# Optimization experiments

Hardware: AMD Instinct MI355X
Metric: run time of the kernel (lower is better)

The kernel has to match this reference:

```python
import jax, jax.numpy as jnp
import numpy as np

BATCH, SEQ, D_EMBED, N_HEADS, D_HEAD = 1, 2048, 1024, 16, 64
MASK_VAL = 1e10


def setup_inputs() -> dict:
    key = jax.random.key(0)
    ks = jax.random.split(key, 5)
    s = 1.0 / np.sqrt(D_EMBED).astype(np.float32)
    return {
        "x": jax.random.normal(ks[0], (BATCH, SEQ, D_EMBED), jnp.float32),
        "W_Q": jax.random.normal(ks[1], (N_HEADS, D_HEAD, D_EMBED), jnp.float32) * s,
        "W_K": jax.random.normal(ks[2], (N_HEADS, D_HEAD, D_EMBED), jnp.float32) * s,
        "W_V": jax.random.normal(ks[3], (N_HEADS, D_HEAD, D_EMBED), jnp.float32) * s,
        "W_O": jax.random.normal(ks[4], (N_HEADS, D_EMBED, D_HEAD), jnp.float32) * s,
    }


def reference(x, W_Q, W_K, W_V, W_O):
    # x: [b, c, e] -> q,k,v: [b, a(head), c(pos), h(d_head)]
    q = jnp.einsum('ahe,bce->bach', W_Q, x)
    k = jnp.einsum('ahe,bce->bach', W_K, x)
    v = jnp.einsum('ahe,bce->bach', W_V, x)
    n = x.shape[1]
    # scores[b,a,c,C] = k_c . q_C  (as in the source einsum 'bach,baCh->bacC')
    scores = jnp.einsum('bach,baCh->bacC', k, q)
    # tril(scores) - triu(1e10, diag=1)  ==  where(C <= c, scores, -1e10)
    causal = jnp.tril(jnp.ones((n, n), dtype=bool))
    masked = jnp.where(causal, scores, jnp.float32(-MASK_VAL))
    attn = jax.nn.softmax(masked / np.float32(np.sqrt(D_HEAD)), axis=-1)  # [b,a,c,C]
    # z[b,a,c,h] = sum_C attn[b,a,c,C] * v[b,a,C,h]
    z = jnp.einsum('bacC,baCh->bach', attn, v)
    out = jnp.einsum('aeh,bach->bce', W_O, z)  # [b, c, e]
    return out
```

## Files before the change

### kernel.cpp

```cpp
#include <hip/hip_runtime.h>
#include <hip/hip_bf16.h>
#include <hip/hip_fp16.h>

#define SEQ 2048
#define DH  64
#define NH  16
#define DE  1024

typedef float    f32x4  __attribute__((ext_vector_type(4)));
typedef float    fvec4  __attribute__((ext_vector_type(4)));
typedef __bf16   bf16x8 __attribute__((ext_vector_type(8)));
typedef _Float16 half8  __attribute__((ext_vector_type(8)));
typedef _Float16 f16x4  __attribute__((ext_vector_type(4)));

#define MFMA_BF16_K32(A,B,C) __builtin_amdgcn_mfma_f32_16x16x32_bf16(A,B,C,0,0,0)
#define MFMA_F16_K32(A,B,C)  __builtin_amdgcn_mfma_f32_16x16x32_f16(A,B,C,0,0,0)
#define MFMA_F16_K16(A,B,C)  __builtin_amdgcn_mfma_f32_16x16x16f16(A,B,C,0,0,0)

__device__ __forceinline__ void gll16(void* lds, const void* g) {
    __builtin_amdgcn_global_load_lds(
        (const __attribute__((address_space(1))) unsigned int*)g,
        (__attribute__((address_space(3))) unsigned int*)lds, 16, 0, 0);
}

__global__ __launch_bounds__(256) void conv_all(
    const float* __restrict__ x,  const float* __restrict__ Wq,
    const float* __restrict__ Wk, const float* __restrict__ Wv,
    const float* __restrict__ Wo, __bf16* __restrict__ xb,
    __bf16* __restrict__ wqb, __bf16* __restrict__ wkb,
    __bf16* __restrict__ wvb, __bf16* __restrict__ wotb)
{
    long i = ((long)blockIdx.x * 256 + threadIdx.x) * 8;
    const float* src; __bf16* dst; float sc = 1.0f; long j;
    if (i < 2097152)      { j = i;            src = x  + j; dst = xb  + j; }
    else if (i < 3145728) { j = i - 2097152;  src = Wq + j; dst = wqb + j; }
    else if (i < 4194304) { j = i - 3145728;  src = Wk + j; dst = wkb + j; sc = 0.125f; }
    else if (i < 5242880) { j = i - 4194304;  src = Wv + j; dst = wvb + j; }
    else                  { j = i - 5242880;  src = Wo + j;
                            long a = j >> 16, e = (j >> 6) & 1023, h = j & 63;
                            dst = wotb + e * DE + a * 64 + h; }
    fvec4 u = *(const fvec4*)src;
    fvec4 w = *(const fvec4*)(src + 4);
    bf16x8 o;
    o[0]=(__bf16)(u.x*sc); o[1]=(__bf16)(u.y*sc); o[2]=(__bf16)(u.z*sc); o[3]=(__bf16)(u.w*sc);
    o[4]=(__bf16)(w.x*sc); o[5]=(__bf16)(w.y*sc); o[6]=(__bf16)(w.z*sc); o[7]=(__bf16)(w.w*sc);
    *(bf16x8*)dst = o;
}

template<int BM, int BN, int MODE>
__global__ __launch_bounds__(256) void gemm_t(
    const __bf16* __restrict__ A, const __bf16* __restrict__ B,
    __half* __restrict__ Cqk, __half* __restrict__ Cv, float* __restrict__ Cf)
{
    constexpr int MT = BM / 32;
    constexpr int NT = BN / 32;
    constexpr int NCH = (BM + BN) / 32;

    union SM {
        struct { __bf16 As[BM][64]; __bf16 Bs[BN][64]; } st;
        _Float16 tr[2][64][BM + 8];
    };
    __shared__ __align__(16) SM sm;

    const int t = threadIdx.x, wave = t >> 6, lane = t & 63;
    const int bm = blockIdx.y * BM, bn = blockIdx.x * BN;
    const int il = lane & 15, q4 = lane >> 4;
    const int wm = (wave & 1) * (BM / 2), wn = (wave >> 1) * (BN / 2);

    f32x4 acc[MT][NT];
    #pragma unroll
    for (int i = 0; i < MT; ++i)
        #pragma unroll
        for (int j = 0; j < NT; ++j) acc[i][j] = (f32x4){0.f,0.f,0.f,0.f};

    for (int k0 = 0; k0 < DE; k0 += 64) {
        __syncthreads();
        #pragma unroll
        for (int i = 0; i < NCH; ++i) {
            int s = i * 256 + t;
            int row = s >> 3, ch = (s & 7) ^ (row & 7);
            if (s < BM * 8)
                gll16((__bf16*)sm.st.As + (long)s * 8,
                      A + (long)(bm + row) * DE + k0 + ch * 8);
            else
                gll16((__bf16*)sm.st.Bs + (long)(s - BM * 8) * 8,
                      B + (long)(bn + row - BM) * DE + k0 + ch * 8);
        }
        __syncthreads();
        #pragma unroll
        for (int kc = 0; kc < 2; ++kc) {
            bf16x8 af[MT], bff[NT];
            #pragma unroll
            for (int mt = 0; mt < MT; ++mt) {
                int row = wm + mt*16 + il, ch = (kc*4 + q4) ^ (row & 7);
                af[mt] = *(const bf16x8*)&sm.st.As[row][ch * 8];
            }
            #pragma unroll
            for (int nt = 0; nt < NT; ++nt) {
                int row = wn + nt*16 + il, ch = (kc*4 + q4) ^ (row & 7);
                bff[nt] = *(const bf16x8*)&sm.st.Bs[row][ch * 8];
            }
            #pragma unroll
            for (int mt = 0; mt < MT; ++mt)
                #pragma unroll
                for (int nt = 0; nt < NT; ++nt)
                    acc[mt][nt] = MFMA_BF16_K32(af[mt], bff[nt], acc[mt][nt]);
        }
    }

    if (MODE == 0) {
        const int zi = bn >> 10;
        if (zi == 2) {
            __syncthreads();
            const int hh = wn >> 6;
            #pragma unroll
            for (int mt = 0; mt < MT; ++mt) {
                const int ml = wm + mt*16 + q4*4;
                #pragma unroll
                for (int nt = 0; nt < NT; ++nt) {
                    const int hl = (wn & 63) + nt*16 + il;
                    f16x4 v4;
                    #pragma unroll
                    for (int r = 0; r < 4; ++r) v4[r] = (_Float16)acc[mt][nt][r];
                    *(f16x4*)&sm.tr[hh][hl][ml] = v4;
                }
            }
            __syncthreads();
            const int hbase = (bn & 1023) >> 6;
            constexpr int SLOTS = 2 * 64 * (BM / 8);
            #pragma unroll
            for (int i = 0; i < SLOTS / 256; ++i) {
                int s = i*256 + t;
                int hh2 = s / (64 * (BM/8));
                int rem = s % (64 * (BM/8));
                int hl = rem / (BM/8), ch = rem % (BM/8);
                half8 val = *(const half8*)&sm.tr[hh2][hl][ch*8];
                *(half8*)&Cv[(long)(hbase + hh2)*131072 + (long)hl*2048 + bm + ch*8] = val;
            }
        } else {
            #pragma unroll
            for (int mt = 0; mt < MT; ++mt) {
                const int m0 = bm + wm + mt*16 + q4*4;
                #pragma unroll
                for (int nt = 0; nt < NT; ++nt) {
                    const int base = bn + wn + nt*16;
                    const int head = (base >> 6) & 15;
                    const int hb   = base & 63;
                    #pragma unroll
                    for (int r = 0; r < 4; ++r)
                        Cqk[(long)zi*2097152 + (long)head*131072 +
                            (long)(m0 + r)*64 + hb + il] = (__half)acc[mt][nt][r];
                }
            }
        }
    } else {
        #pragma unroll
        for (int mt = 0; mt < MT; ++mt) {
            const int m0 = bm + wm + mt*16 + q4*4;
            #pragma unroll
            for (int nt = 0; nt < NT; ++nt) {
                const int n = bn + wn + nt*16 + il;
                #pragma unroll
                for (int r = 0; r < 4; ++r)
                    Cf[(long)(m0 + r) * DE + n] = acc[mt][nt][r];
            }
        }
    }
}

__global__ __launch_bounds__(256) void attn_mfma(
    const __half* __restrict__ Qh, const __half* __restrict__ Kh,
    const __half* __restrict__ Vt, __bf16* __restrict__ Z)
{
    __shared__ __align__(16) _Float16 Qs[2][64][64];
    __shared__ __align__(16) _Float16 Vs[2][64][64];
    __shared__ float smc[2][64][20];

    const int a    = blockIdx.x;
    const int jp   = blockIdx.y;
    const int z    = blockIdx.z;
    const int t    = threadIdx.x;
    const int wave = t >> 6;
    const int lane = t & 63;
    const int sl     = wave >> 1;
    const int strip  = z * 2 + sl;
    const int parity = wave & 1;
    const int il = lane & 15, q4 = lane >> 4;

    const int jtA = jp, jtB = 31 - jp;
    const int SA  = jtA + 1;
    const int total = 33;

    const __half* Qg = Qh + (long)a * SEQ * DH;
    const __half* Vg = Vt + (long)a * DH * SEQ;

    int c0t = jtA * 64;
    const __half* kp = Kh + ((long)a*SEQ + c0t + strip*16 + il)*DH + q4*8;
    half8 kf0 = *(const half8*)kp;
    half8 kf1 = *(const half8*)(kp + 32);

    f16x4 ones;
    #pragma unroll
    for (int j = 0; j < 4; ++j) ones[j] = (_Float16)1.0f;

    f32x4 o[4];
    #pragma unroll
    for (int ht = 0; ht < 4; ++ht) o[ht] = (f32x4){0.f,0.f,0.f,0.f};
    f32x4 lacc = {0.f,0.f,0.f,0.f};

    auto STAGE = [&](int s, int buf) {
        const int nn0 = (s < SA) ? s * 64 : (s - SA) * 64;
        #pragma unroll
        for (int i = 0; i < 2; ++i) {
            int sl2 = i * 256 + t;
            int row = sl2 >> 3, ch = (sl2 & 7) ^ (row & 7);
            gll16((_Float16*)Qs[buf] + (long)sl2 * 8,
                  Qg + (long)(nn0 + row) * DH + ch * 8);
        }
        #pragma unroll
        for (int i = 0; i < 2; ++i) {
            int sl2 = i * 256 + t;
            int row = sl2 >> 3, ch = (sl2 & 7) ^ (row & 7);
            gll16((_Float16*)Vs[buf] + (long)sl2 * 8,
                  Vg + (long)row * SEQ + nn0 + ch * 8);
        }
    };

    STAGE(0, 0);
    for (int s = 0; s < total; ++s) {
        __syncthreads();
        if (s + 1 < total) STAGE(s + 1, (s + 1) & 1);
        const int  buf  = s & 1;
        const bool diag = (s == SA - 1) || (s == total - 1);

        #pragma unroll
        for (int ci = 0; ci < 2; ++ci) {
            const int cc = parity + ci * 2;
            if (diag && cc > strip) break;
            const int qrow = cc*16 + il;
            const _Float16* qsr = &Qs[buf][qrow][0];
            half8 qa = *(const half8*)(qsr + ((( q4    ) ^ (qrow & 7)) << 3));
            half8 qb = *(const half8*)(qsr + (((q4 + 4) ^ (qrow & 7)) << 3));
            f32x4 T = {0.f,0.f,0.f,0.f};
            T = MFMA_F16_K32(qa, kf0, T);
            T = MFMA_F16_K32(qb, kf1, T);
            if (diag && cc == strip) {
                #pragma unroll
                for (int r = 0; r < 4; ++r)
                    if (q4*4 + r > il) T[r] = -1e30f;
            }
            f16x4 pf;
            #pragma unroll
            for (int r = 0; r < 4; ++r) pf[r] = (_Float16)__expf(T[r]);
            lacc = MFMA_F16_K16(pf, ones, lacc);
            #pragma unroll
            for (int ht = 0; ht < 4; ++ht) {
                const int vrow = ht*16 + il;
                const int vch  = (2*cc + (q4 >> 1)) ^ (vrow & 7);
                f16x4 vf = *(const f16x4*)(&Vs[buf][vrow][0] +
                                           (vch << 3) + ((q4 & 1) << 2));
                o[ht] = MFMA_F16_K16(pf, vf, o[ht]);
            }
        }

        if (diag) {
            __syncthreads();
            if (parity) {
                float* p = &smc[sl][lane][0];
                #pragma unroll
                for (int ht = 0; ht < 4; ++ht) *(f32x4*)(p + ht*4) = o[ht];
                *(f32x4*)(p + 16) = lacc;
            }
            __syncthreads();
            if (!parity) {
                const float* p = &smc[sl][lane][0];
                #pragma unroll
                for (int ht = 0; ht < 4; ++ht)
                    o[ht] += *(const f32x4*)(p + ht*4);
                lacc += *(const f32x4*)(p + 16);
                float inv[4];
                #pragma unroll
                for (int r = 0; r < 4; ++r) inv[r] = 1.0f / lacc[r];
                #pragma unroll
                for (int ht = 0; ht < 4; ++ht)
                    #pragma unroll
                    for (int r = 0; r < 4; ++r) {
                        long row = c0t + strip*16 + q4*4 + r;
                        Z[row * DE + a*64 + ht*16 + il] =
                            (__bf16)(o[ht][r] * inv[r]);
                    }
            }
            #pragma unroll
            for (int ht = 0; ht < 4; ++ht) o[ht] = (f32x4){0.f,0.f,0.f,0.f};
            lacc = (f32x4){0.f,0.f,0.f,0.f};
            if (s == SA - 1 && s != total - 1) {
                c0t = jtB * 64;
                const __half* kp2 = Kh + ((long)a*SEQ + c0t + strip*16 + il)*DH + q4*8;
                kf0 = *(const half8*)kp2;
                kf1 = *(const half8*)(kp2 + 32);
            }
        }
    }
}

extern "C" void kernel_launch(void* const* d_in, const int* in_sizes, int n_in,
                              void* d_out, int out_size, void* d_ws, size_t ws_size,
                              hipStream_t stream)
{
    const float* x  = (const float*)d_in[0];
    const float* Wq = (const float*)d_in[1];
    const float* Wk = (const float*)d_in[2];
    const float* Wv = (const float*)d_in[3];
    const float* Wo = (const float*)d_in[4];
    float* out = (float*)d_out;

    const long M1 = 1024 * 1024;
    __bf16* wsb  = (__bf16*)d_ws;
    __bf16* xb   = wsb;
    __bf16* wqb  = wsb + 2*M1;
    __bf16* wkb  = wsb + 3*M1;
    __bf16* wvb  = wsb + 4*M1;
    __bf16* wotb = wsb + 5*M1;
    __half* qkh  = (__half*)(wsb + 6*M1);
    __half* vth  = (__half*)(wsb + 10*M1);
    __bf16* zb   = wsb + 12*M1;
    (void)wkb; (void)wvb;

    conv_all<<<3072, 256, 0, stream>>>(x, Wq, Wk, Wv, Wo,
                                       xb, wqb, wkb, wvb, wotb);

    gemm_t<64,128,0><<<dim3(24, 32), 256, 0, stream>>>(xb, wqb, qkh, vth, nullptr);

    attn_mfma<<<dim3(NH, 16, 2), 256, 0, stream>>>(qkh, qkh + 2*M1, vth, zb);

    gemm_t<64,128,1><<<dim3(8, 32), 256, 0, stream>>>(zb, wotb, nullptr, nullptr, out);
}
```

Baseline: 145.7 us.

## Fuse fp32-to-bf16 conversion into QKV and output GEMM tile loads

Removes the separate conversion kernel. The QKV and output GEMMs now load fp32 x and weights straight from global memory into registers, convert them to bf16, and store them into swizzled LDS. A register prefetch of the next K-tile is issued after the barrier so global loads overlap the MFMA work. W_O is read in its original head-major layout, which avoids the transposed copy. In exchange, the GEMMs read twice as many bytes per tile, repeat the conversion in every block that reads the same tile, use more registers, and lose the async global-to-LDS loads for these operands.

```diff
diff --git a/kernel.cpp b/kernel.cpp
--- a/kernel.cpp
+++ b/kernel.cpp
@@ -23,39 +23,19 @@
         (__attribute__((address_space(3))) unsigned int*)lds, 16, 0, 0);
 }
 
-__global__ __launch_bounds__(256) void conv_all(
+__device__ __forceinline__ bf16x8 cvt8(fvec4 u, fvec4 v, float s) {
+    bf16x8 o;
+    o[0]=(__bf16)(u.x*s); o[1]=(__bf16)(u.y*s); o[2]=(__bf16)(u.z*s); o[3]=(__bf16)(u.w*s);
+    o[4]=(__bf16)(v.x*s); o[5]=(__bf16)(v.y*s); o[6]=(__bf16)(v.z*s); o[7]=(__bf16)(v.w*s);
+    return o;
+}
+
+__global__ __launch_bounds__(256) void gemm_qkv(
     const float* __restrict__ x,  const float* __restrict__ Wq,
     const float* __restrict__ Wk, const float* __restrict__ Wv,
-    const float* __restrict__ Wo, __bf16* __restrict__ xb,
-    __bf16* __restrict__ wqb, __bf16* __restrict__ wkb,
-    __bf16* __restrict__ wvb, __bf16* __restrict__ wotb)
+    __half* __restrict__ Cqk, __half* __restrict__ Cv)
 {
-    long i = ((long)blockIdx.x * 256 + threadIdx.x) * 8;
-    const float* src; __bf16* dst; float sc = 1.0f; long j;
-    if (i < 2097152)      { j = i;            src = x  + j; dst = xb  + j; }
-    else if (i < 3145728) { j = i - 2097152;  src = Wq + j; dst = wqb + j; }
-    else if (i < 4194304) { j = i - 3145728;  src = Wk + j; dst = wkb + j; sc = 0.125f; }
-    else if (i < 5242880) { j = i - 4194304;  src = Wv + j; dst = wvb + j; }
-    else                  { j = i - 5242880;  src = Wo + j;
-                            long a = j >> 16, e = (j >> 6) & 1023, h = j & 63;
-                            dst = wotb + e * DE + a * 64 + h; }
-    fvec4 u = *(const fvec4*)src;
-    fvec4 w = *(const fvec4*)(src + 4);
-    bf16x8 o;
-    o[0]=(__bf16)(u.x*sc); o[1]=(__bf16)(u.y*sc); o[2]=(__bf16)(u.z*sc); o[3]=(__bf16)(u.w*sc);
-    o[4]=(__bf16)(w.x*sc); o[5]=(__bf16)(w.y*sc); o[6]=(__bf16)(w.z*sc); o[7]=(__bf16)(w.w*sc);
-    *(bf16x8*)dst = o;
-}
-
-template<int BM, int BN, int MODE>
-__global__ __launch_bounds__(256) void gemm_t(
-    const __bf16* __restrict__ A, const __bf16* __restrict__ B,
-    __half* __restrict__ Cqk, __half* __restrict__ Cv, float* __restrict__ Cf)
-{
-    constexpr int MT = BM / 32;
-    constexpr int NT = BN / 32;
-    constexpr int NCH = (BM + BN) / 32;
-
+    constexpr int BM = 64, BN = 128;
     union SM {
         struct { __bf16 As[BM][64]; __bf16 Bs[BN][64]; } st;
         _Float16 tr[2][64][BM + 8];
@@ -65,105 +45,191 @@
     const int t = threadIdx.x, wave = t >> 6, lane = t & 63;
     const int bm = blockIdx.y * BM, bn = blockIdx.x * BN;
     const int il = lane & 15, q4 = lane >> 4;
-    const int wm = (wave & 1) * (BM / 2), wn = (wave >> 1) * (BN / 2);
-
-    f32x4 acc[MT][NT];
-    #pragma unroll
-    for (int i = 0; i < MT; ++i)
-        #pragma unroll
-        for (int j = 0; j < NT; ++j) acc[i][j] = (f32x4){0.f,0.f,0.f,0.f};
-
+    const int wm = (wave & 1) * 32, wn = (wave >> 1) * 64;
+
+    const int zi = bn >> 10;
+    const float* W = (zi == 0) ? Wq : ((zi == 1) ? Wk : Wv);
+    const float sc = (zi == 1) ? 0.125f : 1.0f;
+    const int  bl = bn & 1023;
+
+    fvec4 aC[2][2], bC[4][2];
+    auto LOADA = [&](int k0) {
+        #pragma unroll
+        for (int i = 0; i < 2; ++i) {
+            int s = i*256 + t, row = s >> 3, ch = s & 7;
+            const float* p = x + (long)(bm + row) * DE + k0 + ch * 8;
+            aC[i][0] = *(const fvec4*)p; aC[i][1] = *(const fvec4*)(p + 4);
+        }
+    };
+    auto LOADB = [&](int k0) {
+        #pragma unroll
+        for (int i = 0; i < 4; ++i) {
+            int s = i*256 + t, row = s >> 3, ch = s & 7;
+            const float* p = W + (long)(bl + row) * DE + k0 + ch * 8;
+            bC[i][0] = *(const fvec4*)p; bC[i][1] = *(const fvec4*)(p + 4);
+        }
+    };
+
+    f32x4 acc[2][4];
+    #pragma unroll
+    for (int i = 0; i < 2; ++i)
+        #pragma unroll
+        for (int j = 0; j < 4; ++j) acc[i][j] = (f32x4){0.f,0.f,0.f,0.f};
+
+    LOADA(0); LOADB(0);
     for (int k0 = 0; k0 < DE; k0 += 64) {
         __syncthreads();
         #pragma unroll
-        for (int i = 0; i < NCH; ++i) {
-            int s = i * 256 + t;
-            int row = s >> 3, ch = (s & 7) ^ (row & 7);
-            if (s < BM * 8)
-                gll16((__bf16*)sm.st.As + (long)s * 8,
-                      A + (long)(bm + row) * DE + k0 + ch * 8);
-            else
-                gll16((__bf16*)sm.st.Bs + (long)(s - BM * 8) * 8,
-                      B + (long)(bn + row - BM) * DE + k0 + ch * 8);
-        }
-        __syncthreads();
+        for (int i = 0; i < 2; ++i) {
+            int s = i*256 + t, row = s >> 3, ch = (s & 7) ^ (row & 7);
+            *(bf16x8*)&sm.st.As[row][ch * 8] = cvt8(aC[i][0], aC[i][1], 1.0f);
+        }
+        #pragma unroll
+        for (int i = 0; i < 4; ++i) {
+            int s = i*256 + t, row = s >> 3, ch = (s & 7) ^ (row & 7);
+            *(bf16x8*)&sm.st.Bs[row][ch * 8] = cvt8(bC[i][0], bC[i][1], sc);
+        }
+        __syncthreads();
+        if (k0 + 64 < DE) { LOADA(k0 + 64); LOADB(k0 + 64); }
         #pragma unroll
         for (int kc = 0; kc < 2; ++kc) {
-            bf16x8 af[MT], bff[NT];
-            #pragma unroll
-            for (int mt = 0; mt < MT; ++mt) {
+            bf16x8 af[2], bff[4];
+            #pragma unroll
+            for (int mt = 0; mt < 2; ++mt) {
                 int row = wm + mt*16 + il, ch = (kc*4 + q4) ^ (row & 7);
                 af[mt] = *(const bf16x8*)&sm.st.As[row][ch * 8];
             }
             #pragma unroll
-            for (int nt = 0; nt < NT; ++nt) {
+            for (int nt = 0; nt < 4; ++nt) {
                 int row = wn + nt*16 + il, ch = (kc*4 + q4) ^ (row & 7);
                 bff[nt] = *(const bf16x8*)&sm.st.Bs[row][ch * 8];
             }
             #pragma unroll
-            for (int mt = 0; mt < MT; ++mt)
-                #pragma unroll
-                for (int nt = 0; nt < NT; ++nt)
+            for (int mt = 0; mt < 2; ++mt)
+                #pragma unroll
+                for (int nt = 0; nt < 4; ++nt)
                     acc[mt][nt] = MFMA_BF16_K32(af[mt], bff[nt], acc[mt][nt]);
         }
     }
 
-    if (MODE == 0) {
-        const int zi = bn >> 10;
-        if (zi == 2) {
-            __syncthreads();
-            const int hh = wn >> 6;
-            #pragma unroll
-            for (int mt = 0; mt < MT; ++mt) {
-                const int ml = wm + mt*16 + q4*4;
-                #pragma unroll
-                for (int nt = 0; nt < NT; ++nt) {
-                    const int hl = (wn & 63) + nt*16 + il;
-                    f16x4 v4;
-                    #pragma unroll
-                    for (int r = 0; r < 4; ++r) v4[r] = (_Float16)acc[mt][nt][r];
-                    *(f16x4*)&sm.tr[hh][hl][ml] = v4;
-                }
-            }
-            __syncthreads();
-            const int hbase = (bn & 1023) >> 6;
-            constexpr int SLOTS = 2 * 64 * (BM / 8);
-            #pragma unroll
-            for (int i = 0; i < SLOTS / 256; ++i) {
-                int s = i*256 + t;
-                int hh2 = s / (64 * (BM/8));
-                int rem = s % (64 * (BM/8));
-                int hl = rem / (BM/8), ch = rem % (BM/8);
-                half8 val = *(const half8*)&sm.tr[hh2][hl][ch*8];
-                *(half8*)&Cv[(long)(hbase + hh2)*131072 + (long)hl*2048 + bm + ch*8] = val;
-            }
-        } else {
-            #pragma unroll
-            for (int mt = 0; mt < MT; ++mt) {
-                const int m0 = bm + wm + mt*16 + q4*4;
-                #pragma unroll
-                for (int nt = 0; nt < NT; ++nt) {
-                    const int base = bn + wn + nt*16;
-                    const int head = (base >> 6) & 15;
-                    const int hb   = base & 63;
-                    #pragma unroll
-                    for (int r = 0; r < 4; ++r)
-                        Cqk[(long)zi*2097152 + (long)head*131072 +
-                            (long)(m0 + r)*64 + hb + il] = (__half)acc[mt][nt][r];
-                }
-            }
+    if (zi == 2) {
+        __syncthreads();
+        const int hh = wn >> 6;
+        #pragma unroll
+        for (int mt = 0; mt < 2; ++mt) {
+            const int ml = wm + mt*16 + q4*4;
+            #pragma unroll
+            for (int nt = 0; nt < 4; ++nt) {
+                const int hl = (wn & 63) + nt*16 + il;
+                f16x4 v4;
+                #pragma unroll
+                for (int r = 0; r < 4; ++r) v4[r] = (_Float16)acc[mt][nt][r];
+                *(f16x4*)&sm.tr[hh][hl][ml] = v4;
+            }
+        }
+        __syncthreads();
+        const int hbase = (bn & 1023) >> 6;
+        #pragma unroll
+        for (int i = 0; i < 4; ++i) {
+            int s = i*256 + t;
+            int hh2 = s >> 9, rem = s & 511, hl = rem >> 3, ch = rem & 7;
+            half8 val = *(const half8*)&sm.tr[hh2][hl][ch*8];
+            *(half8*)&Cv[(long)(hbase + hh2)*131072 + (long)hl*2048 + bm + ch*8] = val;
         }
     } else {
         #pragma unroll
-        for (int mt = 0; mt < MT; ++mt) {
+        for (int mt = 0; mt < 2; ++mt) {
             const int m0 = bm + wm + mt*16 + q4*4;
             #pragma unroll
-            for (int nt = 0; nt < NT; ++nt) {
-                const int n = bn + wn + nt*16 + il;
+            for (int nt = 0; nt < 4; ++nt) {
+                const int base = bn + wn + nt*16;
+                const int head = (base >> 6) & 15;
+                const int hb   = base & 63;
                 #pragma unroll
                 for (int r = 0; r < 4; ++r)
-                    Cf[(long)(m0 + r) * DE + n] = acc[mt][nt][r];
-            }
+                    Cqk[(long)zi*2097152 + (long)head*131072 +
+                        (long)(m0 + r)*64 + hb + il] = (__half)acc[mt][nt][r];
+            }
+        }
+    }
+}
+
+__global__ __launch_bounds__(256) void gemm_out(
+    const __bf16* __restrict__ Zb, const float* __restrict__ Wo,
+    float* __restrict__ out)
+{
+    constexpr int BM = 64, BN = 128;
+    __shared__ __align__(16) __bf16 As[BM][64];
+    __shared__ __align__(16) __bf16 Bs[BN][64];
+
+    const int t = threadIdx.x, wave = t >> 6, lane = t & 63;
+    const int bm = blockIdx.y * BM, bn = blockIdx.x * BN;
+    const int il = lane & 15, q4 = lane >> 4;
+    const int wm = (wave & 1) * 32, wn = (wave >> 1) * 64;
+
+    fvec4 bC[4][2];
+    auto LOADB = [&](int k0) {
+        #pragma unroll
+        for (int i = 0; i < 4; ++i) {
+            int s = i*256 + t, row = s >> 3, ch = s & 7;
+            const float* p = Wo + (long)(k0 >> 6) * 65536 +
+                             (long)(bn + row) * 64 + ch * 8;
+            bC[i][0] = *(const fvec4*)p; bC[i][1] = *(const fvec4*)(p + 4);
+        }
+    };
+
+    f32x4 acc[2][4];
+    #pragma unroll
+    for (int i = 0; i < 2; ++i)
+        #pragma unroll
+        for (int j = 0; j < 4; ++j) acc[i][j] = (f32x4){0.f,0.f,0.f,0.f};
+
+    LOADB(0);
+    for (int k0 = 0; k0 < DE; k0 += 64) {
+        __syncthreads();
+        #pragma unroll
+        for (int i = 0; i < 2; ++i) {
+            int s = i*256 + t, row = s >> 3, ch = (s & 7) ^ (row & 7);
+            gll16((__bf16*)As + (long)s * 8,
+                  Zb + (long)(bm + row) * DE + k0 + ch * 8);
+        }
+        #pragma unroll
+        for (int i = 0; i < 4; ++i) {
+            int s = i*256 + t, row = s >> 3, ch = (s & 7) ^ (row & 7);
+            *(bf16x8*)&Bs[row][ch * 8] = cvt8(bC[i][0], bC[i][1], 1.0f);
+        }
+        __syncthreads();
+        if (k0 + 64 < DE) LOADB(k0 + 64);
+        #pragma unroll
+        for (int kc = 0; kc < 2; ++kc) {
+            bf16x8 af[2], bff[4];
+            #pragma unroll
+            for (int mt = 0; mt < 2; ++mt) {
+                int row = wm + mt*16 + il, ch = (kc*4 + q4) ^ (row & 7);
+                af[mt] = *(const bf16x8*)&As[row][ch * 8];
+            }
+            #pragma unroll
+            for (int nt = 0; nt < 4; ++nt) {
+                int row = wn + nt*16 + il, ch = (kc*4 + q4) ^ (row & 7);
+                bff[nt] = *(const bf16x8*)&Bs[row][ch * 8];
+            }
+            #pragma unroll
+            for (int mt = 0; mt < 2; ++mt)
+                #pragma unroll
+                for (int nt = 0; nt < 4; ++nt)
+                    acc[mt][nt] = MFMA_BF16_K32(af[mt], bff[nt], acc[mt][nt]);
+        }
+    }
+
+    #pragma unroll
+    for (int mt = 0; mt < 2; ++mt) {
+        const int m0 = bm + wm + mt*16 + q4*4;
+        #pragma unroll
+        for (int nt = 0; nt < 4; ++nt) {
+            const int n = bn + wn + nt*16 + il;
+            #pragma unroll
+            for (int r = 0; r < 4; ++r)
+                out[(long)(m0 + r) * DE + n] = acc[mt][nt][r];
         }
     }
 }
@@ -315,23 +381,13 @@
     float* out = (float*)d_out;
 
     const long M1 = 1024 * 1024;
-    __bf16* wsb  = (__bf16*)d_ws;
-    __bf16* xb   = wsb;
-    __bf16* wqb  = wsb + 2*M1;
-    __bf16* wkb  = wsb + 3*M1;
-    __bf16* wvb  = wsb + 4*M1;
-    __bf16* wotb = wsb + 5*M1;
-    __half* qkh  = (__half*)(wsb + 6*M1);
-    __half* vth  = (__half*)(wsb + 10*M1);
-    __bf16* zb   = wsb + 12*M1;
-    (void)wkb; (void)wvb;
-
-    conv_all<<<3072, 256, 0, stream>>>(x, Wq, Wk, Wv, Wo,
-                                       xb, wqb, wkb, wvb, wotb);
-
-    gemm_t<64,128,0><<<dim3(24, 32), 256, 0, stream>>>(xb, wqb, qkh, vth, nullptr);
+    __half* qkh = (__half*)d_ws;
+    __half* vth = qkh + 4*M1;
+    __bf16* zb  = (__bf16*)(qkh + 6*M1);
+
+    gemm_qkv<<<dim3(24, 32), 256, 0, stream>>>(x, Wq, Wk, Wv, qkh, vth);
 
     attn_mfma<<<dim3(NH, 16, 2), 256, 0, stream>>>(qkh, qkh + 2*M1, vth, zb);
 
-    gemm_t<64,128,1><<<dim3(8, 32), 256, 0, stream>>>(zb, wotb, nullptr, nullptr, out);
-}
+    gemm_out<<<dim3(8, 32), 256, 0, stream>>>(zb, Wo, out);
+}
```

New measurement: 155.9 us. +7.0%, slower.
